# Kernel optimization log

Measured on AMD Instinct MI355X. Metric: run time of the kernel, lower is better.

The kernel has to match this reference:

```python
import jax, jax.numpy as jnp
import numpy as np

K = 3          # kernel_size
STRIDE = 1
PAD = 1
BASIS = 8      # act_fun.get_size() (Hermite basis order)


def _unfold(x):
    # x: [B, Cin, H, W] -> patches [B, Cin, K*K, L] (same ordering as F.unfold)
    b, c, h, w = x.shape
    p = jax.lax.conv_general_dilated_patches(
        x, filter_shape=(K, K), window_strides=(STRIDE, STRIDE),
        padding=[(PAD, PAD), (PAD, PAD)])
    # p: [B, Cin*K*K, Hout, Wout], channel-major ordering (Cin, Kh, Kw)
    ho, wo = p.shape[2], p.shape[3]
    return p.reshape(b, c, K * K, ho * wo), ho, wo


def _hermite(x):
    # Physicists' Hermite polynomials H_0..H_{BASIS-1}, stacked on last axis.
    hs = [jnp.ones_like(x), 2.0 * x]
    for n in range(1, BASIS - 1):
        hs.append(2.0 * x * hs[n] - 2.0 * n * hs[n - 1])
    return jnp.stack(hs[:BASIS], axis=-1)


def setup_inputs() -> dict:
    key = jax.random.key(0)
    k1, k2, k3, k4 = jax.random.split(key, 4)
    cin, cout = 64, 128
    x = jax.random.normal(k1, (16, cin, 32, 32), dtype=jnp.float32)
    # xavier_normal on [Cin,Cout,K^2,1]: std = sqrt(2/(fan_in+fan_out)) over last two dims -> use small randn
    w_b = jax.random.normal(k2, (cin, cout, K * K, 1), dtype=jnp.float32)
    w_s = jax.random.normal(k3, (cin, cout, K * K, 1), dtype=jnp.float32) * 0.001
    c = jax.random.normal(k4, (cin, cout, K * K, 1, BASIS), dtype=jnp.float32) * 0.1
    return {"x": x, "w_b": w_b, "w_s": w_s, "c": c}


def reference(x, w_b, w_s, c):
    b = x.shape[0]
    xw, ho, wo = _unfold(x)                      # [B, Cin, K2, L]
    phi = _hermite(xw)                           # [B, Cin, K2, L, BASIS]
    res = jax.nn.silu(xw)                        # residual activation
    # effective spline weight: w_s * c, contracted over Cin, K2, basis
    cw = w_s[..., 0, None] * c[:, :, :, 0, :]    # [Cin, Cout, K2, BASIS]
    out = (jnp.einsum('ioka,bikla->bol', cw, phi)
           + jnp.einsum('iok,bikl->bol', w_b[..., 0], res))  # [B, Cout, L]
    return out.reshape(b, -1, ho, wo)
```

## Files before the change

### kernel.cpp

```cpp
#include <hip/hip_runtime.h>
#include <stdint.h>

typedef unsigned short ushort_t;
typedef short short8 __attribute__((ext_vector_type(8)));
typedef float f32x4 __attribute__((ext_vector_type(4)));

#define CIN   64
#define COUT  128
#define BATCH 16
#define LPIX  1024
#define NTOT  (BATCH*LPIX)
#define C2N   576
#define PIXN  (BATCH*34*34)
#define NSTEP2 72
#define KS    4
#define PART_ELEMS (NTOT*COUT)
#define FEAT_BLOCKS (PIXN/4)
#define WPREP_BLOCKS 128

#define FEAT_BYTES (PIXN*C2N*2)
#define W_OFF      FEAT_BYTES
#define W_BYTES    (COUT*NSTEP2*64*2)
#define BIAS_OFF   (W_OFF + W_BYTES)
#define PART_OFF   (BIAS_OFF + 512)
#define PART_BYTES (PART_ELEMS*2)
#define WS_NEED    ((size_t)PART_OFF + (size_t)KS*PART_BYTES)

#define VM0() asm volatile("s_waitcnt vmcnt(0)" ::: "memory")
#define BAR() __builtin_amdgcn_s_barrier()

__device__ __forceinline__ ushort_t to_bf16(float f) {
  union { float f; uint32_t u; } v; v.f = f;
  uint32_t r = (v.u + 0x7fffu + ((v.u >> 16) & 1u)) >> 16;
  return (ushort_t)r;
}
__device__ __forceinline__ float from_bf16(ushort_t u) {
  union { uint32_t u; float f; } v; v.u = ((uint32_t)u) << 16;
  return v.f;
}

__device__ __forceinline__ void basis9(float x, float* o) {
  float hm = 1.f, h = 2.f * x;
  o[0] = hm; o[1] = h;
#pragma unroll
  for (int n = 1; n < 7; ++n) {
    float nx = 2.f * x * h - 2.f * (float)n * hm;
    hm = h; h = nx;
    o[n + 1] = nx;
  }
  o[8] = x / (1.f + __expf(-x));
}

__device__ __forceinline__ void load16(const void* g, void* l) {
  __builtin_amdgcn_global_load_lds(
      (const __attribute__((address_space(1))) uint32_t*)g,
      (__attribute__((address_space(3))) uint32_t*)l, 16, 0, 0);
}

__global__ void prep_kernel(const float* __restrict__ x, ushort_t* __restrict__ feat,
                            const float* __restrict__ wb, const float* __restrict__ wsp,
                            const float* __restrict__ cc, ushort_t* __restrict__ W,
                            float* __restrict__ bias) {
  const int t = threadIdx.x;
  if (blockIdx.x < WPREP_BLOCKS) {
    __shared__ ushort_t wl[NSTEP2 * 64];
    const int m = blockIdx.x;
    if (t < 64) {
      const int i = t;
      const int base = (i * COUT + m) * 9;
      const int r = ((((i >> 3) & 7) ^ (m & 7)) << 3) | (i & 7);
      float h0 = 0.f;
#pragma unroll
      for (int kk = 0; kk < 9; ++kk) {
        const float ws_ = wsp[base + kk];
        const float wbv = wb[base + kk];
        const float* cp = cc + (size_t)(base + kk) * 8;
        h0 += ws_ * cp[0];
#pragma unroll
        for (int sf = 1; sf <= 8; ++sf) {
          const float val = (sf < 8) ? ws_ * cp[sf] : wbv;
          wl[((sf - 1) * 9 + kk) * 64 + r] = to_bf16(val);
        }
      }
#pragma unroll
      for (int off = 32; off > 0; off >>= 1) h0 += __shfl_down(h0, off, 64);
      if (t == 0) bias[m] = h0;
    }
    __syncthreads();
    uint32_t* dst = (uint32_t*)&W[(size_t)m * (NSTEP2 * 64)];
    const uint32_t* src = (const uint32_t*)wl;
#pragma unroll
    for (int jj = 0; jj < 9; ++jj) dst[jj * 256 + t] = src[jj * 256 + t];
  } else {
    const int lane = t & 63;
    const int pg = (blockIdx.x - WPREP_BLOCKS) * 4 + (t >> 6);
    const int xx = pg % 34;
    const int rest = pg / 34;
    const int yy = rest % 34;
    const int bb = rest / 34;
    float v = 0.f;
    if (xx >= 1 && xx <= 32 && yy >= 1 && yy <= 32)
      v = x[((bb * CIN + lane) * 32 + (yy - 1)) * 32 + (xx - 1)];
    float o[9];
    basis9(v, o);
    ushort_t* dst = feat + (size_t)pg * C2N + lane;
#pragma unroll
    for (int f = 1; f < 9; ++f) dst[f * 64] = to_bf16(o[f]);
  }
}

__global__ __launch_bounds__(256, 2) void gemm_kernel(const ushort_t* __restrict__ feat,
                                                      const ushort_t* __restrict__ W,
                                                      ushort_t* __restrict__ part) {
  __shared__ ushort_t Ab[4][4096];
  __shared__ ushort_t Hb[2720 * 8];
  const int t = threadIdx.x;
  const int lane = t & 63;
  const int wn = t >> 6;

  const int logical = (blockIdx.x & 7) * 64 + (blockIdx.x >> 3);
  const int nb = logical >> 3;
  const int rem = logical & 7;
  const int mt = rem >> 2;
  const int ksplit = rem & 3;
  const int lo = ksplit * 18;

  const int b  = nb >> 2;
  const int y0 = (nb & 3) * 8;
  const int pixbase = (b * 34 + y0) * 34;

  const char* Wb = (const char*)W + mt * 64 * (NSTEP2 * 64 * 2);
  const char* Fb = (const char*)feat;

  f32x4 acc[4][4];
#pragma unroll
  for (int a = 0; a < 4; ++a)
#pragma unroll
    for (int c = 0; c < 4; ++c) acc[a][c] = (f32x4)0.f;

  auto stage_halo = [&](int c2s) {
    const char* base = Fb + (size_t)pixbase * (C2N * 2) + (c2s + 1) * 128;
#pragma unroll
    for (int it = 0; it < 11; ++it) {
      const int q = it * 256 + t;
      if (q < 2720) {
        const int L = q >> 3;
        const int sl = (q & 7) ^ (L & 7);
        load16(base + L * (C2N * 2) + (sl << 4), &Hb[q * 8]);
      }
    }
  };

  auto stageA = [&](int p, int s) {
#pragma unroll
    for (int q = 0; q < 2; ++q) {
      const int idx16 = q * 256 + t;
      const int m = idx16 >> 3, ccn = idx16 & 7;
      load16(Wb + m * (NSTEP2 * 64 * 2) + s * 128 + ccn * 16, &Ab[p][idx16 * 8]);
    }
  };

  auto compute = [&](int p, int j) {
    const int dy = j / 3, dx = j - dy * 3;
#pragma unroll
    for (int ks = 0; ks < 2; ++ks) {
      short8 av[4], bv[4];
      const int kslot = ks * 4 + (lane >> 4);
#pragma unroll
      for (int mf = 0; mf < 4; ++mf) {
        const int row = mf * 16 + (lane & 15);
        av[mf] = *(const short8*)&Ab[p][row * 64 + ((kslot ^ (row & 7)) << 3)];
      }
#pragma unroll
      for (int nf = 0; nf < 4; ++nf) {
        const int nl = wn * 64 + nf * 16 + (lane & 15);
        const int L = ((nl >> 5) + dy) * 34 + (nl & 31) + dx;
        bv[nf] = *(const short8*)&Hb[L * 64 + ((kslot ^ (L & 7)) << 3)];
      }
      __builtin_amdgcn_s_setprio(1);
#pragma unroll
      for (int mf = 0; mf < 4; ++mf)
#pragma unroll
        for (int nf = 0; nf < 4; ++nf)
          acc[mf][nf] = __builtin_amdgcn_mfma_f32_16x16x32_bf16(av[mf], bv[nf],
                                                                acc[mf][nf], 0, 0, 0);
      __builtin_amdgcn_s_setprio(0);
    }
  };

  stage_halo(2 * ksplit);
  stageA(0, lo + 0);
  stageA(1, lo + 1);

  VM0(); BAR(); stageA(2, lo + 2);  stageA(3, lo + 3);  compute(0, 0); compute(1, 1);
  VM0(); BAR(); stageA(0, lo + 4);  stageA(1, lo + 5);  compute(2, 2); compute(3, 3);
  VM0(); BAR(); stageA(2, lo + 6);  stageA(3, lo + 7);  compute(0, 4); compute(1, 5);
  VM0(); BAR(); stageA(0, lo + 8);  stageA(1, lo + 9);  compute(2, 6); compute(3, 7);
  VM0(); BAR();                                         compute(0, 8);
  BAR(); stage_halo(2 * ksplit + 1); stageA(2, lo + 10);
  VM0(); BAR(); stageA(3, lo + 11); stageA(0, lo + 12); compute(1, 0); compute(2, 1);
  VM0(); BAR(); stageA(1, lo + 13); stageA(2, lo + 14); compute(3, 2); compute(0, 3);
  VM0(); BAR(); stageA(3, lo + 15); stageA(0, lo + 16); compute(1, 4); compute(2, 5);
  VM0(); BAR(); stageA(1, lo + 17);                     compute(3, 6); compute(0, 7);
  VM0(); BAR();                                         compute(1, 8);

  ushort_t* dst = part + (size_t)ksplit * PART_ELEMS;
#pragma unroll
  for (int mf = 0; mf < 4; ++mf)
#pragma unroll
    for (int rg = 0; rg < 4; ++rg) {
      const int m = mt * 64 + mf * 16 + (lane >> 4) * 4 + rg;
#pragma unroll
      for (int nf = 0; nf < 4; ++nf) {
        const int n = nb * 256 + wn * 64 + nf * 16 + (lane & 15);
        const int bb = n >> 10, ll = n & 1023;
        __builtin_nontemporal_store(to_bf16(acc[mf][nf][rg]),
                                    &dst[(bb * COUT + m) * LPIX + ll]);
      }
    }
}

__global__ void add_kernel(float* __restrict__ out, const ushort_t* __restrict__ part,
                           const float* __restrict__ bias) {
  const int i = (blockIdx.x * 256 + threadIdx.x) * 8;
  const float bv = bias[(i >> 10) & 127];
  f32x4 a0 = (f32x4)bv;
  f32x4 a1 = (f32x4)bv;
#pragma unroll
  for (int j = 0; j < KS; ++j) {
    const short8 pv = __builtin_nontemporal_load(
        (const short8*)&part[(size_t)j * PART_ELEMS + i]);
#pragma unroll
    for (int e = 0; e < 4; ++e) {
      a0[e] += from_bf16((ushort_t)pv[e]);
      a1[e] += from_bf16((ushort_t)pv[e + 4]);
    }
  }
  __builtin_nontemporal_store(a0, (f32x4*)&out[i]);
  __builtin_nontemporal_store(a1, (f32x4*)&out[i + 4]);
}

__global__ void naive_kernel(const float* __restrict__ x, const float* __restrict__ wb,
                             const float* __restrict__ wsp, const float* __restrict__ cc,
                             float* __restrict__ out) {
  const int idx = blockIdx.x * 256 + threadIdx.x;
  if (idx >= BATCH * COUT * LPIX) return;
  const int l = idx & 1023, o = (idx >> 10) & 127, b = idx >> 17;
  const int h = l >> 5, w = l & 31;
  float acc = 0.f;
  for (int i = 0; i < CIN; ++i)
    for (int kk = 0; kk < 9; ++kk) {
      const int yy = h + kk / 3 - 1, xx = w + kk % 3 - 1;
      const float v = (yy >= 0 && yy < 32 && xx >= 0 && xx < 32)
                          ? x[((b * CIN + i) * 32 + yy) * 32 + xx] : 0.f;
      float ftr[9];
      basis9(v, ftr);
      const int base = (i * COUT + o) * 9 + kk;
      const float* cp = cc + base * 8;
      float dot = 0.f;
#pragma unroll
      for (int f = 0; f < 8; ++f) dot += cp[f] * ftr[f];
      acc += wsp[base] * dot + wb[base] * ftr[8];
    }
  out[idx] = acc;
}

extern "C" void kernel_launch(void* const* d_in, const int* in_sizes, int n_in,
                              void* d_out, int out_size, void* d_ws, size_t ws_size,
                              hipStream_t stream) {
  const float* x  = (const float*)d_in[0];
  const float* wb = (const float*)d_in[1];
  const float* wsp = (const float*)d_in[2];
  const float* cc = (const float*)d_in[3];
  float* out = (float*)d_out;

  if (ws_size < WS_NEED) {
    naive_kernel<<<(BATCH * COUT * LPIX + 255) / 256, 256, 0, stream>>>(x, wb, wsp, cc, out);
    return;
  }

  char* ws = (char*)d_ws;
  ushort_t* feat = (ushort_t*)ws;
  ushort_t* W    = (ushort_t*)(ws + W_OFF);
  float* bias    = (float*)(ws + BIAS_OFF);
  ushort_t* part = (ushort_t*)(ws + PART_OFF);

  prep_kernel<<<WPREP_BLOCKS + FEAT_BLOCKS, 256, 0, stream>>>(x, feat, wb, wsp, cc, W, bias);
  gemm_kernel<<<64 * 2 * KS, 256, 0, stream>>>(feat, W, part);
  add_kernel<<<PART_ELEMS / 2048, 256, 0, stream>>>(out, part, bias);
}
```

Before: 39.15 us.

## Replace split-K partial buffers and add kernel with float atomics into output

The add kernel and the bf16 partial-sum buffers are removed. The prep kernel now also zeroes the output, and each split-K GEMM block adds its fp32 accumulators directly into the output with hardware float atomic adds. Split 0 also adds the bias. This saves one kernel launch plus the write and read-back of four partial tensors, at the cost of atomic traffic to L2 and a non-deterministic summation order.

```diff
diff --git a/kernel.cpp b/kernel.cpp
--- a/kernel.cpp
+++ b/kernel.cpp
@@ -14,17 +14,16 @@
 #define PIXN  (BATCH*34*34)
 #define NSTEP2 72
 #define KS    4
-#define PART_ELEMS (NTOT*COUT)
+#define OUT_ELEMS (NTOT*COUT)
 #define FEAT_BLOCKS (PIXN/4)
 #define WPREP_BLOCKS 128
+#define ZERO_BLOCKS 1024
 
 #define FEAT_BYTES (PIXN*C2N*2)
 #define W_OFF      FEAT_BYTES
 #define W_BYTES    (COUT*NSTEP2*64*2)
 #define BIAS_OFF   (W_OFF + W_BYTES)
-#define PART_OFF   (BIAS_OFF + 512)
-#define PART_BYTES (PART_ELEMS*2)
-#define WS_NEED    ((size_t)PART_OFF + (size_t)KS*PART_BYTES)
+#define WS_NEED    ((size_t)BIAS_OFF + 512)
 
 #define VM0() asm volatile("s_waitcnt vmcnt(0)" ::: "memory")
 #define BAR() __builtin_amdgcn_s_barrier()
@@ -33,10 +32,6 @@
   union { float f; uint32_t u; } v; v.f = f;
   uint32_t r = (v.u + 0x7fffu + ((v.u >> 16) & 1u)) >> 16;
   return (ushort_t)r;
-}
-__device__ __forceinline__ float from_bf16(ushort_t u) {
-  union { uint32_t u; float f; } v; v.u = ((uint32_t)u) << 16;
-  return v.f;
 }
 
 __device__ __forceinline__ void basis9(float x, float* o) {
@@ -60,7 +55,7 @@
 __global__ void prep_kernel(const float* __restrict__ x, ushort_t* __restrict__ feat,
                             const float* __restrict__ wb, const float* __restrict__ wsp,
                             const float* __restrict__ cc, ushort_t* __restrict__ W,
-                            float* __restrict__ bias) {
+                            float* __restrict__ bias, float* __restrict__ out) {
   const int t = threadIdx.x;
   if (blockIdx.x < WPREP_BLOCKS) {
     __shared__ ushort_t wl[NSTEP2 * 64];
@@ -91,7 +86,7 @@
     const uint32_t* src = (const uint32_t*)wl;
 #pragma unroll
     for (int jj = 0; jj < 9; ++jj) dst[jj * 256 + t] = src[jj * 256 + t];
-  } else {
+  } else if (blockIdx.x < WPREP_BLOCKS + FEAT_BLOCKS) {
     const int lane = t & 63;
     const int pg = (blockIdx.x - WPREP_BLOCKS) * 4 + (t >> 6);
     const int xx = pg % 34;
@@ -106,12 +101,18 @@
     ushort_t* dst = feat + (size_t)pg * C2N + lane;
 #pragma unroll
     for (int f = 1; f < 9; ++f) dst[f * 64] = to_bf16(o[f]);
+  } else {
+    const int zb = blockIdx.x - (WPREP_BLOCKS + FEAT_BLOCKS);
+    f32x4* dst = (f32x4*)out + (size_t)zb * 512 + t;
+    dst[0] = (f32x4)0.f;
+    dst[256] = (f32x4)0.f;
   }
 }
 
 __global__ __launch_bounds__(256, 2) void gemm_kernel(const ushort_t* __restrict__ feat,
                                                       const ushort_t* __restrict__ W,
-                                                      ushort_t* __restrict__ part) {
+                                                      const float* __restrict__ bias,
+                                                      float* __restrict__ out) {
   __shared__ ushort_t Ab[4][4096];
   __shared__ ushort_t Hb[2720 * 8];
   const int t = threadIdx.x;
@@ -204,40 +205,19 @@
   VM0(); BAR(); stageA(1, lo + 17);                     compute(3, 6); compute(0, 7);
   VM0(); BAR();                                         compute(1, 8);
 
-  ushort_t* dst = part + (size_t)ksplit * PART_ELEMS;
 #pragma unroll
   for (int mf = 0; mf < 4; ++mf)
 #pragma unroll
     for (int rg = 0; rg < 4; ++rg) {
       const int m = mt * 64 + mf * 16 + (lane >> 4) * 4 + rg;
+      const float bv = (ksplit == 0) ? bias[m] : 0.f;
 #pragma unroll
       for (int nf = 0; nf < 4; ++nf) {
         const int n = nb * 256 + wn * 64 + nf * 16 + (lane & 15);
         const int bb = n >> 10, ll = n & 1023;
-        __builtin_nontemporal_store(to_bf16(acc[mf][nf][rg]),
-                                    &dst[(bb * COUT + m) * LPIX + ll]);
-      }
-    }
-}
-
-__global__ void add_kernel(float* __restrict__ out, const ushort_t* __restrict__ part,
-                           const float* __restrict__ bias) {
-  const int i = (blockIdx.x * 256 + threadIdx.x) * 8;
-  const float bv = bias[(i >> 10) & 127];
-  f32x4 a0 = (f32x4)bv;
-  f32x4 a1 = (f32x4)bv;
-#pragma unroll
-  for (int j = 0; j < KS; ++j) {
-    const short8 pv = __builtin_nontemporal_load(
-        (const short8*)&part[(size_t)j * PART_ELEMS + i]);
-#pragma unroll
-    for (int e = 0; e < 4; ++e) {
-      a0[e] += from_bf16((ushort_t)pv[e]);
-      a1[e] += from_bf16((ushort_t)pv[e + 4]);
-    }
-  }
-  __builtin_nontemporal_store(a0, (f32x4*)&out[i]);
-  __builtin_nontemporal_store(a1, (f32x4*)&out[i + 4]);
+        unsafeAtomicAdd(&out[(bb * COUT + m) * LPIX + ll], acc[mf][nf][rg] + bv);
+      }
+    }
 }
 
 __global__ void naive_kernel(const float* __restrict__ x, const float* __restrict__ wb,
@@ -283,9 +263,8 @@
   ushort_t* feat = (ushort_t*)ws;
   ushort_t* W    = (ushort_t*)(ws + W_OFF);
   float* bias    = (float*)(ws + BIAS_OFF);
-  ushort_t* part = (ushort_t*)(ws + PART_OFF);
-
-  prep_kernel<<<WPREP_BLOCKS + FEAT_BLOCKS, 256, 0, stream>>>(x, feat, wb, wsp, cc, W, bias);
-  gemm_kernel<<<64 * 2 * KS, 256, 0, stream>>>(feat, W, part);
-  add_kernel<<<PART_ELEMS / 2048, 256, 0, stream>>>(out, part, bias);
-}
+
+  prep_kernel<<<WPREP_BLOCKS + FEAT_BLOCKS + ZERO_BLOCKS, 256, 0, stream>>>(
+      x, feat, wb, wsp, cc, W, bias, out);
+  gemm_kernel<<<64 * 2 * KS, 256, 0, stream>>>(feat, W, bias, out);
+}
```

After: 54.85 us. 1.4x slower.
